# Kernel optimization log

Hardware: AMD Instinct MI355X
Metric: run time of the kernel (lower is better)

## Reference

```python
import jax, jax.numpy as jnp
import numpy as np

B, S, D, H, HD = 2, 2048, 1024, 16, 64


def setup_inputs() -> dict:
    key = jax.random.key(0)
    ks = jax.random.split(key, 5)
    sc = 1.0 / np.sqrt(D)  # lecun-normal-ish scale for kernels
    return {
        "x": jax.random.normal(ks[0], (B, S, D), jnp.float32),
        "Wq": jax.random.normal(ks[1], (D, H, HD), jnp.float32) * sc,
        "bq": jnp.zeros((H, HD), jnp.float32),
        "Wk": jax.random.normal(ks[2], (D, H, HD), jnp.float32) * sc,
        "bk": jnp.zeros((H, HD), jnp.float32),
        "Wv": jax.random.normal(ks[3], (D, H, HD), jnp.float32) * sc,
        "bv": jnp.zeros((H, HD), jnp.float32),
        "Wo": jax.random.normal(ks[4], (H, HD, D), jnp.float32) * (1.0 / np.sqrt(H * HD)),
        "bo": jnp.zeros((D,), jnp.float32),
    }


def reference(x, Wq, bq, Wk, bk, Wv, bv, Wo, bo):
    # QKV projections: [B,S,D] x [D,H,Hd] -> [B,S,H,Hd]
    q = jnp.einsum("bsd,dhk->bshk", x, Wq) + bq
    k = jnp.einsum("bsd,dhk->bshk", x, Wk) + bk
    v = jnp.einsum("bsd,dhk->bshk", x, Wv) + bv
    depth = q.shape[-1]
    q = q / jnp.sqrt(jnp.asarray(depth, q.dtype))
    # attention weights [B,H,Sq,Sk]
    attn = jnp.einsum("bqhd,bkhd->bhqk", q, k)
    attn = jax.nn.softmax(attn, axis=-1)
    # weighted values [B,Sq,H,Hd]
    out = jnp.einsum("bhqk,bkhd->bqhd", attn, v)
    # output projection back to d_model
    return jnp.einsum("bqhd,hdm->bqm", out, Wo) + bo
```

## Files before the change

### kernel.cpp

```cpp
#include <hip/hip_runtime.h>


typedef __attribute__((ext_vector_type(8))) short short8;
typedef __attribute__((ext_vector_type(4))) float float4v;
typedef __attribute__((ext_vector_type(16))) float f32x16;
typedef __attribute__((ext_vector_type(2))) int int2v;

__device__ __forceinline__ void async16(void* lds, const void* g) {
  __builtin_amdgcn_global_load_lds(
      (__attribute__((address_space(1))) void*)(g),
      (__attribute__((address_space(3))) void*)(lds), 16, 0, 0);
}

__device__ __forceinline__ short f2bf(float f) {
  union { float f; unsigned u; } v;
  v.f = f;
  unsigned r = v.u + 0x7fffu + ((v.u >> 16) & 1u);
  return (short)(r >> 16);
}

#if __has_builtin(__builtin_amdgcn_cvt_pk_bf16_f32)
__device__ __forceinline__ unsigned pk2(float a, float b) {
  auto h = __builtin_amdgcn_cvt_pk_bf16_f32(a, b);
  unsigned u;
  __builtin_memcpy(&u, &h, 4);
  return u;
}
#else
__device__ __forceinline__ unsigned pk2(float a, float b) {
  return (unsigned)(unsigned short)f2bf(a) |
         ((unsigned)(unsigned short)f2bf(b) << 16);
}
#endif

#if __has_builtin(__builtin_amdgcn_exp2f)
__device__ __forceinline__ float fexp2(float x) { return __builtin_amdgcn_exp2f(x); }
#else
__device__ __forceinline__ float fexp2(float x) { return exp2f(x); }
#endif

__device__ __forceinline__ void plswap(unsigned& a, unsigned& b) {
#if __has_builtin(__builtin_amdgcn_permlane32_swap)
  int2v r = __builtin_amdgcn_permlane32_swap((int)a, (int)b, false, false);
  a = (unsigned)r[0];
  b = (unsigned)r[1];
#else
  unsigned ax = (unsigned)__shfl_xor((int)a, 32);
  unsigned bx = (unsigned)__shfl_xor((int)b, 32);
  bool hh = (threadIdx.x & 32) != 0;
  a = hh ? bx : a;
  b = hh ? b : ax;
#endif
}

__device__ __forceinline__ short8 mk8(unsigned a, unsigned b, unsigned c,
                                      unsigned d) {
  union { unsigned u[4]; short8 s; } r;
  r.u[0] = a; r.u[1] = b; r.u[2] = c; r.u[3] = d;
  return r.s;
}

__device__ __forceinline__ short8 cvt8(const float* __restrict__ g) {
  float4v a = *(const float4v*)(g);
  float4v b = *(const float4v*)(g + 4);
  union { unsigned u[4]; short8 s; } r;
  r.u[0] = pk2(a[0], a[1]);
  r.u[1] = pk2(a[2], a[3]);
  r.u[2] = pk2(b[0], b[1]);
  r.u[3] = pk2(b[2], b[3]);
  return r.s;
}

__device__ __forceinline__ void mfma_tile(const short* As, const short* Bs,
                                          float4v acc[4][4]) {
  int t = threadIdx.x, lane = t & 63, w = t >> 6, r = lane & 15, q = lane >> 4;
  int wr = (w >> 1) * 64, wc = (w & 1) * 64;
  short8 af[4], bfr[4];
#pragma unroll
  for (int mt = 0; mt < 4; mt++)
    af[mt] = *(const short8*)(As + (wr + mt * 16 + r) * 32 + q * 8);
#pragma unroll
  for (int nt = 0; nt < 4; nt++)
    bfr[nt] = *(const short8*)(Bs + (wc + nt * 16 + r) * 32 + q * 8);
#pragma unroll
  for (int mt = 0; mt < 4; mt++)
#pragma unroll
    for (int nt = 0; nt < 4; nt++)
      acc[mt][nt] = __builtin_amdgcn_mfma_f32_16x16x32_bf16(
          af[mt], bfr[nt], acc[mt][nt], 0, 0, 0);
}

__global__ __launch_bounds__(256) void convw_t3(
    const float* __restrict__ W0, const float* __restrict__ W1,
    const float* __restrict__ W2, short* __restrict__ dst) {
  __shared__ short tile[64][65];
  int z = blockIdx.z;
  const float* src = (z == 0) ? W0 : (z == 1) ? W1 : W2;
  short* d = dst + z * 1048576;
  int r0 = blockIdx.y * 64, c0 = blockIdx.x * 64;
  int t = threadIdx.x;
#pragma unroll
  for (int i = 0; i < 16; i++) {
    int e = i * 256 + t;
    int r = e >> 6, c = e & 63;
    tile[r][c] = f2bf(src[(r0 + r) * 1024 + c0 + c]);
  }
  __syncthreads();
#pragma unroll
  for (int i = 0; i < 16; i++) {
    int e = i * 256 + t;
    int r = e >> 6, c = e & 63;
    d[(c0 + r) * 1024 + r0 + c] = tile[c][r];
  }
}

__global__ __launch_bounds__(256) void convwo_t(
    const float* __restrict__ W, short* __restrict__ d) {
  __shared__ short tile[64][65];
  int r0 = blockIdx.y * 64, c0 = blockIdx.x * 64;
  int t = threadIdx.x;
#pragma unroll
  for (int i = 0; i < 16; i++) {
    int e = i * 256 + t;
    int r = e >> 6, c = e & 63;
    tile[r][c] = f2bf(W[(r0 + r) * 1024 + c0 + c]);
  }
  __syncthreads();
#pragma unroll
  for (int i = 0; i < 16; i++) {
    int e = i * 256 + t;
    int r = e >> 6, c = e & 63;
    d[(c0 + r) * 1024 + r0 + c] = tile[c][r];
  }
}

__global__ __launch_bounds__(256) void conv_x(
    const float* __restrict__ x, short* __restrict__ xb) {
  int i = (blockIdx.x * 256 + threadIdx.x) * 8;
  *(short8*)(xb + i) = cvt8(x + i);
}

__global__ __launch_bounds__(256, 2) void qkv_gemm_fast(
    const short* __restrict__ xb, const short* __restrict__ WT,
    const float* __restrict__ bq, const float* __restrict__ bk,
    const float* __restrict__ bv, short* __restrict__ Qd,
    short* __restrict__ Kd, short* __restrict__ Vt0, short* __restrict__ Vt1) {
  __shared__ __align__(16) short As[4096];
  __shared__ __align__(16) short Bs[4096];
  int z = blockIdx.z;
  int t = threadIdx.x;
  int m0, n0;
  if (z < 2) { m0 = blockIdx.y * 128; n0 = blockIdx.x * 128; }
  else       { m0 = blockIdx.x * 128; n0 = blockIdx.y * 128; }
  const short* Wz = WT + z * 1048576;
  const short* A = (z < 2) ? xb : Wz;
  const short* B = (z < 2) ? Wz : xb;
  float4v acc[4][4];
#pragma unroll
  for (int mt = 0; mt < 4; mt++)
#pragma unroll
    for (int nt = 0; nt < 4; nt++)
#pragma unroll
      for (int k = 0; k < 4; k++) acc[mt][nt][k] = 0.0f;

  for (int kt = 0; kt < 32; kt++) {
    int k0 = kt * 32;
    __syncthreads();
#pragma unroll
    for (int i = 0; i < 2; i++) {
      int p = i * 256 + t;
      int rr = p >> 2, cc = p & 3;
      async16(As + p * 8, A + (m0 + rr) * 1024 + k0 + cc * 8);
      async16(Bs + p * 8, B + (n0 + rr) * 1024 + k0 + cc * 8);
    }
    __syncthreads();
    mfma_tile(As, Bs, acc);
  }
  int lane = t & 63, w = t >> 6, r = lane & 15, q = lane >> 4;
  int wr = (w >> 1) * 64, wc = (w & 1) * 64;
  if (z < 2) {
    const float* bias = (z == 0) ? bq : bk;
    short* dst = (z == 0) ? Qd : Kd;
    float scale = (z == 0) ? 0.1803368801111204f : 1.0f;
#pragma unroll
    for (int mt = 0; mt < 4; mt++)
#pragma unroll
      for (int reg = 0; reg < 4; reg++) {
        int m = m0 + wr + mt * 16 + q * 4 + reg;
        int b = m >> 11, s = m & 2047;
#pragma unroll
        for (int nt = 0; nt < 4; nt++) {
          int n = n0 + wc + nt * 16 + r;
          int h = n >> 6, hd = n & 63;
          float v = (acc[mt][nt][reg] + bias[n]) * scale;
          dst[((b * 16 + h) << 17) + (s << 6) + hd] = f2bf(v);
        }
      }
  } else {
#pragma unroll
    for (int mt = 0; mt < 4; mt++)
#pragma unroll
      for (int reg = 0; reg < 4; reg++) {
        int mrow = m0 + wr + mt * 16 + q * 4 + reg;
        int h = mrow >> 6, hd = mrow & 63;
        float bias = bv[mrow];
#pragma unroll
        for (int nt = 0; nt < 4; nt++) {
          int n = n0 + wc + nt * 16 + r;
          int b = n >> 11, s = n & 2047;
          int idx = b * 16 + h;
          short* vp = (idx < 16) ? (Vt0 + idx * 131072)
                                 : (Vt1 + (idx - 16) * 131072);
          vp[(hd << 11) + s] = f2bf(acc[mt][nt][reg] + bias);
        }
      }
  }
}

__device__ __forceinline__ void stage_kv(short* Ksb, short* Vsb,
                                         const short* Kt, const short* Vt,
                                         int t) {
#pragma unroll
  for (int i = 0; i < 2; i++) {
    int p = i * 256 + t, rr = p >> 3, c = p & 7, cs = (c ^ (rr & 7)) * 8;
    async16(Ksb + p * 8, Kt + rr * 64 + cs);
    async16(Vsb + p * 8, Vt + rr * 2048 + cs);
  }
}

__global__ __launch_bounds__(256, 4) void attn_kernel(
    short* __restrict__ QO, const short* __restrict__ K,
    const short* __restrict__ V0, const short* __restrict__ V1) {
  __shared__ __align__(16) short SM[16640];
  float* sums = (float*)(SM + 16384);
  float* xl = (float*)(SM + 16512);
  float* xo = (float*)SM;
  int id = blockIdx.x;
  int chunk = id >> 3;
  int bh = (id & 7) * 4 + (chunk >> 5);
  int qt = chunk & 31;
  int t = threadIdx.x, lane = t & 63, w = t >> 6;
  int l31 = lane & 31, hi = lane >> 5;
  int qsel = w & 1, kh = w >> 1;
  short* Qb = QO + bh * 131072;
  const short* Kb = K + bh * 131072;
  const short* Vb = (bh < 16) ? (V0 + bh * 131072) : (V1 + (bh - 16) * 131072);
  int q0w = qt * 64 + qsel * 32;

  short8 qf[4];
#pragma unroll
  for (int ds = 0; ds < 4; ds++)
    qf[ds] = *(const short8*)(Qb + (q0w + l31) * 64 + ds * 16 + hi * 8);

  f32x16 oacc[2];
#pragma unroll
  for (int ht = 0; ht < 2; ht++)
#pragma unroll
    for (int i = 0; i < 16; i++) oacc[ht][i] = 0.0f;
  float lsum = 0.0f;

  stage_kv(SM, SM + 8192, Kb, Vb, t);
  __syncthreads();

  for (int kt = 0; kt < 32; kt++) {
    int cur = kt & 1;
    if (kt < 31)
      stage_kv(SM + (cur ^ 1) * 4096, SM + 8192 + (cur ^ 1) * 4096,
               Kb + (kt + 1) * 4096, Vb + (kt + 1) * 64, t);
    const short* Kc = SM + cur * 4096;
    const short* Vc = SM + 8192 + cur * 4096;
    {
      int ck = kh;
      int kr = ck * 32 + l31;
      short8 ka[4];
#pragma unroll
      for (int ds = 0; ds < 4; ds++)
        ka[ds] =
            *(const short8*)(Kc + kr * 64 + (((ds * 2 + hi) ^ (kr & 7)) * 8));
      f32x16 sacc;
#pragma unroll
      for (int i = 0; i < 16; i++) sacc[i] = 0.0f;
      __builtin_amdgcn_s_setprio(1);
#pragma unroll
      for (int ds = 0; ds < 4; ds++)
        sacc = __builtin_amdgcn_mfma_f32_32x32x16_bf16(ka[ds], qf[ds], sacc,
                                                       0, 0, 0);
      __builtin_amdgcn_s_setprio(0);
      float pv[16];
#pragma unroll
      for (int i = 0; i < 16; i++) pv[i] = fexp2(sacc[i]);
      lsum += (((pv[0] + pv[1]) + (pv[2] + pv[3])) +
               ((pv[4] + pv[5]) + (pv[6] + pv[7]))) +
              (((pv[8] + pv[9]) + (pv[10] + pv[11])) +
               ((pv[12] + pv[13]) + (pv[14] + pv[15])));
      unsigned u0 = pk2(pv[0], pv[1]), u1 = pk2(pv[2], pv[3]);
      unsigned u2 = pk2(pv[4], pv[5]), u3 = pk2(pv[6], pv[7]);
      unsigned u4 = pk2(pv[8], pv[9]), u5 = pk2(pv[10], pv[11]);
      unsigned u6 = pk2(pv[12], pv[13]), u7 = pk2(pv[14], pv[15]);
      plswap(u0, u2);
      plswap(u1, u3);
      plswap(u4, u6);
      plswap(u5, u7);
      short8 pa[2];
      pa[0] = mk8(u0, u1, u2, u3);
      pa[1] = mk8(u4, u5, u6, u7);
#pragma unroll
      for (int ks = 0; ks < 2; ks++) {
        short8 vb8[2];
#pragma unroll
        for (int ht = 0; ht < 2; ht++) {
          int d = ht * 32 + l31;
          vb8[ht] = *(const short8*)(Vc + d * 64 +
                                     (((ck * 4 + ks * 2 + hi) ^ (d & 7)) * 8));
        }
        __builtin_amdgcn_s_setprio(1);
#pragma unroll
        for (int ht = 0; ht < 2; ht++)
          oacc[ht] = __builtin_amdgcn_mfma_f32_32x32x16_bf16(
              pa[ks], vb8[ht], oacc[ht], 0, 0, 0);
        __builtin_amdgcn_s_setprio(0);
      }
    }
    __syncthreads();
  }

  float lt = lsum + __shfl_xor(lsum, 32);
  float* xb = xo + (qsel * 64 + lane) * 33;
  if (kh == 1) {
#pragma unroll
    for (int i = 0; i < 16; i++) xb[i] = oacc[0][i];
#pragma unroll
    for (int i = 0; i < 16; i++) xb[16 + i] = oacc[1][i];
    if (lane < 32) xl[qsel * 32 + l31] = lt;
  }
  __syncthreads();
  if (kh == 0) {
#pragma unroll
    for (int i = 0; i < 16; i++) oacc[0][i] += xb[i];
#pragma unroll
    for (int i = 0; i < 16; i++) oacc[1][i] += xb[16 + i];
    float ltot = lt + xl[qsel * 32 + l31];
    float inv = 1.0f / fmaxf(ltot, 1.0e-30f);
    if (lane < 32) sums[qsel * 32 + l31] = inv;
    __builtin_amdgcn_s_waitcnt(0xC07F);
#pragma unroll
    for (int rg = 0; rg < 16; rg++) {
      int srow = (rg & 3) + 8 * (rg >> 2) + 4 * hi;
      float invr = sums[qsel * 32 + srow];
      short* orow = Qb + (q0w + srow) * 64;
      orow[l31] = f2bf(oacc[0][rg] * invr);
      orow[32 + l31] = f2bf(oacc[1][rg] * invr);
    }
  }
}

__global__ __launch_bounds__(256, 2) void out_gemm(
    const short* __restrict__ O, const short* __restrict__ WoT,
    const float* __restrict__ bo, float* __restrict__ out) {
  __shared__ __align__(16) short As[4096];
  __shared__ __align__(16) short Bs[2048];
  int m0 = blockIdx.y * 128, n0 = blockIdx.x * 64;
  int t = threadIdx.x, lane = t & 63, w = t >> 6, r = lane & 15, q = lane >> 4;
  int wr = (w >> 1) * 64, wc = (w & 1) * 32;
  float4v acc[4][2];
#pragma unroll
  for (int mt = 0; mt < 4; mt++)
#pragma unroll
    for (int nt = 0; nt < 2; nt++)
#pragma unroll
      for (int k = 0; k < 4; k++) acc[mt][nt][k] = 0.0f;

  for (int kt = 0; kt < 32; kt++) {
    int k0 = kt * 32;
    int h0 = k0 >> 6, hd0 = k0 & 63;
    __syncthreads();
#pragma unroll
    for (int i = 0; i < 2; i++) {
      int p = i * 256 + t;
      int rr = p >> 2, cc = p & 3;
      int m = m0 + rr;
      async16(As + p * 8, O + (m >> 11) * 2097152 + h0 * 131072 +
                              (m & 2047) * 64 + hd0 + cc * 8);
    }
    {
      int rr = t >> 2, cc = t & 3;
      async16(Bs + t * 8, WoT + (n0 + rr) * 1024 + k0 + cc * 8);
    }
    __syncthreads();
    short8 af[4], bfr[2];
#pragma unroll
    for (int mt = 0; mt < 4; mt++)
      af[mt] = *(const short8*)(As + (wr + mt * 16 + r) * 32 + q * 8);
#pragma unroll
    for (int nt = 0; nt < 2; nt++)
      bfr[nt] = *(const short8*)(Bs + (wc + nt * 16 + r) * 32 + q * 8);
#pragma unroll
    for (int mt = 0; mt < 4; mt++)
#pragma unroll
      for (int nt = 0; nt < 2; nt++)
        acc[mt][nt] = __builtin_amdgcn_mfma_f32_16x16x32_bf16(
            af[mt], bfr[nt], acc[mt][nt], 0, 0, 0);
  }
#pragma unroll
  for (int mt = 0; mt < 4; mt++)
#pragma unroll
    for (int reg = 0; reg < 4; reg++) {
      int m = m0 + wr + mt * 16 + q * 4 + reg;
#pragma unroll
      for (int nt = 0; nt < 2; nt++) {
        int n = n0 + wc + nt * 16 + r;
        out[m * 1024 + n] = acc[mt][nt][reg] + bo[n];
      }
    }
}

extern "C" void kernel_launch(void* const* d_in, const int* in_sizes, int n_in,
                              void* d_out, int out_size, void* d_ws,
                              size_t ws_size, hipStream_t stream) {
  (void)in_sizes; (void)n_in; (void)out_size; (void)ws_size;
  const float* x = (const float*)d_in[0];
  const float* Wq = (const float*)d_in[1];
  const float* bq = (const float*)d_in[2];
  const float* Wk = (const float*)d_in[3];
  const float* bk = (const float*)d_in[4];
  const float* Wv = (const float*)d_in[5];
  const float* bv = (const float*)d_in[6];
  const float* Wo = (const float*)d_in[7];
  const float* bo = (const float*)d_in[8];
  float* out = (float*)d_out;
  char* ws = (char*)d_ws;
  short* QO  = (short*)(ws);
  short* Kws = (short*)(ws + (8u << 20));
  short* WoT = (short*)(ws + (8u << 20));
  short* xb  = (short*)d_out;
  short* WT  = (short*)d_out + 4 * 1048576;
  short* Vt0 = (short*)Wq;
  short* Vt1 = (short*)Wk;

  dim3 tb(256);
  convw_t3<<<dim3(16, 16, 3), tb, 0, stream>>>(Wq, Wk, Wv, WT);
  conv_x<<<dim3(2048), tb, 0, stream>>>(x, xb);
  qkv_gemm_fast<<<dim3(8, 32, 3), tb, 0, stream>>>(xb, WT, bq, bk, bv,
                                                   QO, Kws, Vt0, Vt1);
  attn_kernel<<<dim3(1024), tb, 0, stream>>>(QO, Kws, Vt0, Vt1);
  convwo_t<<<dim3(16, 16), tb, 0, stream>>>(Wo, WoT);
  out_gemm<<<dim3(16, 32), tb, 0, stream>>>(QO, WoT, bo, out);
}
```

Baseline: 202.4 us.

## Software-pipeline attention softmax across K tiles and merge conversion kernels

The attention loop is restructured so the QK^T MFMAs for tile kt run alongside the exp/pack and PV MFMAs for tile kt-1. Two score accumulators ping-pong, V fragments are preloaded into registers before the barrier, and a prologue and epilogue handle the first and last tiles. This aims to hide exp and LDS-read latency behind matrix work. Separately, the x conversion and the Wq/Wk/Wv transpose-conversion kernels are merged into one launch to save a launch. The pipelining raises register pressure at 4 waves per SIMD occupancy.

```diff
diff --git a/kernel.cpp b/kernel.cpp
--- a/kernel.cpp
+++ b/kernel.cpp
@@ -90,15 +90,24 @@
           af[mt], bfr[nt], acc[mt][nt], 0, 0, 0);
 }
 
-__global__ __launch_bounds__(256) void convw_t3(
+__global__ __launch_bounds__(256) void conv_wx(
     const float* __restrict__ W0, const float* __restrict__ W1,
-    const float* __restrict__ W2, short* __restrict__ dst) {
+    const float* __restrict__ W2, const float* __restrict__ x,
+    short* __restrict__ WT, short* __restrict__ xb) {
   __shared__ short tile[64][65];
-  int z = blockIdx.z;
+  int b = blockIdx.x;
+  int t = threadIdx.x;
+  if (b < 2048) {
+    int i = (b * 256 + t) * 8;
+    *(short8*)(xb + i) = cvt8(x + i);
+    return;
+  }
+  int wb = b - 2048;
+  int z = wb >> 8;
+  int rem = wb & 255;
   const float* src = (z == 0) ? W0 : (z == 1) ? W1 : W2;
-  short* d = dst + z * 1048576;
-  int r0 = blockIdx.y * 64, c0 = blockIdx.x * 64;
-  int t = threadIdx.x;
+  short* d = WT + z * 1048576;
+  int r0 = (rem >> 4) * 64, c0 = (rem & 15) * 64;
 #pragma unroll
   for (int i = 0; i < 16; i++) {
     int e = i * 256 + t;
@@ -132,12 +141,6 @@
     int r = e >> 6, c = e & 63;
     d[(c0 + r) * 1024 + r0 + c] = tile[c][r];
   }
-}
-
-__global__ __launch_bounds__(256) void conv_x(
-    const float* __restrict__ x, short* __restrict__ xb) {
-  int i = (blockIdx.x * 256 + threadIdx.x) * 8;
-  *(short8*)(xb + i) = cvt8(x + i);
 }
 
 __global__ __launch_bounds__(256, 2) void qkv_gemm_fast(
@@ -227,6 +230,58 @@
     async16(Vsb + p * 8, Vt + rr * 2048 + cs);
   }
 }
+
+#define ATTN_BODY(FIRST, LAST, KT, SIN, SOUT)                                 \
+  {                                                                           \
+    if (!(LAST))                                                              \
+      stage_kv(SM + (((KT) + 1) & 1) * 4096,                                  \
+               SM + 8192 + (((KT) + 1) & 1) * 4096, Kb + ((KT) + 1) * 4096,   \
+               Vb + ((KT) + 1) * 64, t);                                      \
+    short8 pa[2];                                                             \
+    if (!(FIRST)) {                                                           \
+      float pvv[16];                                                          \
+      _Pragma("unroll") for (int i = 0; i < 16; i++) pvv[i] = fexp2(SIN[i]);  \
+      lsum += (((pvv[0] + pvv[1]) + (pvv[2] + pvv[3])) +                      \
+               ((pvv[4] + pvv[5]) + (pvv[6] + pvv[7]))) +                     \
+              (((pvv[8] + pvv[9]) + (pvv[10] + pvv[11])) +                    \
+               ((pvv[12] + pvv[13]) + (pvv[14] + pvv[15])));                  \
+      unsigned u0 = pk2(pvv[0], pvv[1]), u1 = pk2(pvv[2], pvv[3]);            \
+      unsigned u2 = pk2(pvv[4], pvv[5]), u3 = pk2(pvv[6], pvv[7]);            \
+      unsigned u4 = pk2(pvv[8], pvv[9]), u5 = pk2(pvv[10], pvv[11]);          \
+      unsigned u6 = pk2(pvv[12], pvv[13]), u7 = pk2(pvv[14], pvv[15]);        \
+      plswap(u0, u2);                                                         \
+      plswap(u1, u3);                                                         \
+      plswap(u4, u6);                                                         \
+      plswap(u5, u7);                                                         \
+      pa[0] = mk8(u0, u1, u2, u3);                                            \
+      pa[1] = mk8(u4, u5, u6, u7);                                            \
+    }                                                                         \
+    const short* Kc = SM + ((KT) & 1) * 4096;                                 \
+    const short* Vc = SM + 8192 + ((KT) & 1) * 4096;                          \
+    int kr = kh * 32 + l31;                                                   \
+    short8 ka[4];                                                             \
+    _Pragma("unroll") for (int ds = 0; ds < 4; ds++) ka[ds] =                 \
+        *(const short8*)(Kc + kr * 64 + (((ds * 2 + hi) ^ (kr & 7)) * 8));    \
+    _Pragma("unroll") for (int i = 0; i < 16; i++) SOUT[i] = 0.0f;            \
+    __builtin_amdgcn_s_setprio(1);                                            \
+    _Pragma("unroll") for (int ds = 0; ds < 4; ds++) SOUT =                   \
+        __builtin_amdgcn_mfma_f32_32x32x16_bf16(ka[ds], qf[ds], SOUT, 0, 0,   \
+                                                0);                           \
+    if (!(FIRST)) {                                                           \
+      _Pragma("unroll") for (int ks = 0; ks < 2; ks++)                        \
+          _Pragma("unroll") for (int ht = 0; ht < 2; ht++) oacc[ht] =         \
+          __builtin_amdgcn_mfma_f32_32x32x16_bf16(pa[ks], vbr[ks * 2 + ht],   \
+                                                  oacc[ht], 0, 0, 0);         \
+    }                                                                         \
+    __builtin_amdgcn_s_setprio(0);                                            \
+    _Pragma("unroll") for (int ks = 0; ks < 2; ks++)                          \
+        _Pragma("unroll") for (int ht = 0; ht < 2; ht++) {                    \
+      int d = ht * 32 + l31;                                                  \
+      vbr[ks * 2 + ht] = *(const short8*)(                                    \
+          Vc + d * 64 + (((kh * 4 + ks * 2 + hi) ^ (d & 7)) * 8));            \
+    }                                                                         \
+    __syncthreads();                                                          \
+  }
 
 __global__ __launch_bounds__(256, 4) void attn_kernel(
     short* __restrict__ QO, const short* __restrict__ K,
@@ -253,6 +308,8 @@
     qf[ds] = *(const short8*)(Qb + (q0w + l31) * 64 + ds * 16 + hi * 8);
 
   f32x16 oacc[2];
+  f32x16 sA, sB;
+  short8 vbr[4];
 #pragma unroll
   for (int ht = 0; ht < 2; ht++)
 #pragma unroll
@@ -262,66 +319,39 @@
   stage_kv(SM, SM + 8192, Kb, Vb, t);
   __syncthreads();
 
-  for (int kt = 0; kt < 32; kt++) {
-    int cur = kt & 1;
-    if (kt < 31)
-      stage_kv(SM + (cur ^ 1) * 4096, SM + 8192 + (cur ^ 1) * 4096,
-               Kb + (kt + 1) * 4096, Vb + (kt + 1) * 64, t);
-    const short* Kc = SM + cur * 4096;
-    const short* Vc = SM + 8192 + cur * 4096;
-    {
-      int ck = kh;
-      int kr = ck * 32 + l31;
-      short8 ka[4];
-#pragma unroll
-      for (int ds = 0; ds < 4; ds++)
-        ka[ds] =
-            *(const short8*)(Kc + kr * 64 + (((ds * 2 + hi) ^ (kr & 7)) * 8));
-      f32x16 sacc;
-#pragma unroll
-      for (int i = 0; i < 16; i++) sacc[i] = 0.0f;
-      __builtin_amdgcn_s_setprio(1);
-#pragma unroll
-      for (int ds = 0; ds < 4; ds++)
-        sacc = __builtin_amdgcn_mfma_f32_32x32x16_bf16(ka[ds], qf[ds], sacc,
-                                                       0, 0, 0);
-      __builtin_amdgcn_s_setprio(0);
-      float pv[16];
-#pragma unroll
-      for (int i = 0; i < 16; i++) pv[i] = fexp2(sacc[i]);
-      lsum += (((pv[0] + pv[1]) + (pv[2] + pv[3])) +
-               ((pv[4] + pv[5]) + (pv[6] + pv[7]))) +
-              (((pv[8] + pv[9]) + (pv[10] + pv[11])) +
-               ((pv[12] + pv[13]) + (pv[14] + pv[15])));
-      unsigned u0 = pk2(pv[0], pv[1]), u1 = pk2(pv[2], pv[3]);
-      unsigned u2 = pk2(pv[4], pv[5]), u3 = pk2(pv[6], pv[7]);
-      unsigned u4 = pk2(pv[8], pv[9]), u5 = pk2(pv[10], pv[11]);
-      unsigned u6 = pk2(pv[12], pv[13]), u7 = pk2(pv[14], pv[15]);
-      plswap(u0, u2);
-      plswap(u1, u3);
-      plswap(u4, u6);
-      plswap(u5, u7);
-      short8 pa[2];
-      pa[0] = mk8(u0, u1, u2, u3);
-      pa[1] = mk8(u4, u5, u6, u7);
-#pragma unroll
-      for (int ks = 0; ks < 2; ks++) {
-        short8 vb8[2];
-#pragma unroll
-        for (int ht = 0; ht < 2; ht++) {
-          int d = ht * 32 + l31;
-          vb8[ht] = *(const short8*)(Vc + d * 64 +
-                                     (((ck * 4 + ks * 2 + hi) ^ (d & 7)) * 8));
-        }
-        __builtin_amdgcn_s_setprio(1);
-#pragma unroll
-        for (int ht = 0; ht < 2; ht++)
-          oacc[ht] = __builtin_amdgcn_mfma_f32_32x32x16_bf16(
-              pa[ks], vb8[ht], oacc[ht], 0, 0, 0);
-        __builtin_amdgcn_s_setprio(0);
-      }
-    }
-    __syncthreads();
+  ATTN_BODY(true, false, 0, sB, sA);
+  for (int kt = 1; kt < 31; kt += 2) {
+    ATTN_BODY(false, false, kt, sA, sB);
+    ATTN_BODY(false, false, kt + 1, sB, sA);
+  }
+  ATTN_BODY(false, true, 31, sA, sB);
+
+  {
+    float pvv[16];
+#pragma unroll
+    for (int i = 0; i < 16; i++) pvv[i] = fexp2(sB[i]);
+    lsum += (((pvv[0] + pvv[1]) + (pvv[2] + pvv[3])) +
+             ((pvv[4] + pvv[5]) + (pvv[6] + pvv[7]))) +
+            (((pvv[8] + pvv[9]) + (pvv[10] + pvv[11])) +
+             ((pvv[12] + pvv[13]) + (pvv[14] + pvv[15])));
+    unsigned u0 = pk2(pvv[0], pvv[1]), u1 = pk2(pvv[2], pvv[3]);
+    unsigned u2 = pk2(pvv[4], pvv[5]), u3 = pk2(pvv[6], pvv[7]);
+    unsigned u4 = pk2(pvv[8], pvv[9]), u5 = pk2(pvv[10], pvv[11]);
+    unsigned u6 = pk2(pvv[12], pvv[13]), u7 = pk2(pvv[14], pvv[15]);
+    plswap(u0, u2);
+    plswap(u1, u3);
+    plswap(u4, u6);
+    plswap(u5, u7);
+    short8 pa0 = mk8(u0, u1, u2, u3);
+    short8 pa1 = mk8(u4, u5, u6, u7);
+#pragma unroll
+    for (int ht = 0; ht < 2; ht++)
+      oacc[ht] = __builtin_amdgcn_mfma_f32_32x32x16_bf16(pa0, vbr[ht],
+                                                         oacc[ht], 0, 0, 0);
+#pragma unroll
+    for (int ht = 0; ht < 2; ht++)
+      oacc[ht] = __builtin_amdgcn_mfma_f32_32x32x16_bf16(pa1, vbr[2 + ht],
+                                                         oacc[ht], 0, 0, 0);
   }
 
   float lt = lsum + __shfl_xor(lsum, 32);
@@ -438,8 +468,7 @@
   short* Vt1 = (short*)Wk;
 
   dim3 tb(256);
-  convw_t3<<<dim3(16, 16, 3), tb, 0, stream>>>(Wq, Wk, Wv, WT);
-  conv_x<<<dim3(2048), tb, 0, stream>>>(x, xb);
+  conv_wx<<<dim3(2816), tb, 0, stream>>>(Wq, Wk, Wv, x, WT, xb);
   qkv_gemm_fast<<<dim3(8, 32, 3), tb, 0, stream>>>(xb, WT, bq, bk, bv,
                                                    QO, Kws, Vt0, Vt1);
   attn_kernel<<<dim3(1024), tb, 0, stream>>>(QO, Kws, Vt0, Vt1);
```

New measurement: 225.4 us. 1.11x slower.
